# Kernel optimization log

Measured on AMD Instinct MI355X. Metric: run time of the kernel, lower is better.

Reference implementation:

```python
import jax, jax.numpy as jnp
import numpy as np

B, T, C = 4, 4096, 1024
DEGREE, EXPAND = 2, 2
H = EXPAND * C  # selector / inner dim = 2048


def setup_inputs() -> dict:
    key = jax.random.key(0)
    ks = jax.random.split(key, 4)
    sc = lambda d: 1.0 / np.sqrt(d)
    return {
        "x": jax.random.normal(ks[0], (B, T, C), jnp.float32),
        "W_sel": jax.random.normal(ks[1], (C, H), jnp.float32) * sc(C),
        "W_agg": jax.random.normal(ks[2], (C, DEGREE * H), jnp.float32) * sc(C),
        "W_out": jax.random.normal(ks[3], (H, C), jnp.float32) * sc(H),
        "sqk_q": jnp.ones((H,), jnp.float32),
        "sqk_k": jnp.ones((DEGREE * H,), jnp.float32),
    }


def reference(x, W_sel, W_agg, W_out, sqk_q, sqk_k):
    # Selector branch on queries (gated): B,T,H
    s = jax.nn.silu(jnp.einsum('btc,ch->bth', x, W_sel) * sqk_q)
    # Aggregator branch on context: B,T,DEGREE*H
    h = jnp.einsum('btc,cd->btd', x, W_agg) * sqk_k
    chunks = jnp.split(h, DEGREE, axis=-1)
    # Polynomial expansion: sum_{d=1..DEGREE} prod_{k<=d} chunk_k  -> B,T,H
    p = chunks[0]
    poly = p
    for c in chunks[1:]:
        p = p * c
        poly = poly + p
    # Causal masked mean: tril(ones(T,T)) @ poly / row-count == cumsum / arange.
    # Honors the causal structure without materializing the T x T mask.
    denom = jnp.arange(1, T + 1, dtype=poly.dtype)[None, :, None]
    agg = jnp.cumsum(poly, axis=1) / denom  # B,T,H causal running mean
    # Mix selected queries with aggregated polynomial state, project out.
    return jnp.einsum('bth,hc->btc', s * agg, W_out)
```

## Files before the change

### kernel.cpp

```cpp
#include <hip/hip_runtime.h>
#include <hip/hip_bf16.h>
#include <stdint.h>

#define BB 4
#define TT 4096
#define CC 1024
#define HH 2048
#define MM (BB*TT)
#define NCK 32
#define CKS 128

using short8 = __attribute__((ext_vector_type(8))) short;
using f32x4  = __attribute__((ext_vector_type(4))) float;

__device__ __forceinline__ unsigned short f2bf(float f) {
    union { float f; uint32_t u; } v; v.f = f;
    uint32_t r = v.u + 0x7fffu + ((v.u >> 16) & 1u);
    return (unsigned short)(r >> 16);
}
__device__ __forceinline__ float bf2f(unsigned short s) {
    union { uint32_t u; float f; } v; v.u = ((uint32_t)s) << 16;
    return v.f;
}
__device__ __forceinline__ float bf_lo(uint32_t u) {
    union { uint32_t u; float f; } v; v.u = u << 16; return v.f;
}
__device__ __forceinline__ float bf_hi(uint32_t u) {
    union { uint32_t u; float f; } v; v.u = u & 0xFFFF0000u; return v.f;
}
__device__ __forceinline__ uint32_t pack2bf(float lo, float hi) {
    return ((uint32_t)f2bf(lo)) | (((uint32_t)f2bf(hi)) << 16);
}

__global__ void conv_x_kernel(const float* __restrict__ x, unsigned short* __restrict__ xb, int n4) {
    int i = blockIdx.x * blockDim.x + threadIdx.x;
    if (i >= n4) return;
    float4 v = ((const float4*)x)[i];
    ushort4 o;
    o.x = f2bf(v.x); o.y = f2bf(v.y); o.z = f2bf(v.z); o.w = f2bf(v.w);
    ((ushort4*)xb)[i] = o;
}

__global__ void trans_direct_kernel(const float* __restrict__ in, unsigned short* __restrict__ out,
                                    const float* __restrict__ scale, int R, int Cin) {
    __shared__ float tile[32][33];
    int c0 = blockIdx.x * 32, k0 = blockIdx.y * 32;
    int tx = threadIdx.x;
    for (int i = threadIdx.y; i < 32; i += 8) {
        float s = scale ? scale[c0 + tx] : 1.f;
        tile[i][tx] = in[(size_t)(k0 + i) * Cin + c0 + tx] * s;
    }
    __syncthreads();
    for (int i = threadIdx.y; i < 32; i += 8)
        out[(size_t)(c0 + i) * R + k0 + tx] = f2bf(tile[tx][i]);
}

__global__ void trans_pair_kernel(const float* __restrict__ in, unsigned short* __restrict__ out,
                                  const float* __restrict__ scale) {
    __shared__ float tile[32][33];
    int q0 = blockIdx.x * 32, k0 = blockIdx.y * 32;
    int g = q0 >> 5;
    int tx = threadIdx.x;
    int c = (tx < 16) ? (g * 16 + tx) : (2048 + g * 16 + tx - 16);
    float s = scale[c];
    for (int i = threadIdx.y; i < 32; i += 8)
        tile[i][tx] = in[(size_t)(k0 + i) * 4096 + c] * s;
    __syncthreads();
    for (int i = threadIdx.y; i < 32; i += 8)
        out[(size_t)(q0 + i) * 1024 + k0 + tx] = f2bf(tile[tx][i]);
}

__global__ __launch_bounds__(256) void gemm_fused_kernel(
    const unsigned short* __restrict__ A,
    const unsigned short* __restrict__ Bt,
    unsigned short* __restrict__ Sout,
    unsigned short* __restrict__ Pout)
{
    __shared__ __align__(16) unsigned short As[128 * 32];
    __shared__ __align__(16) unsigned short Bs[128 * 32];

    const int mt = blockIdx.x / 48;
    const int nt = blockIdx.x % 48;
    const int m0 = mt << 7, n0 = nt << 7;

    const int tid  = threadIdx.x;
    const int lane = tid & 63;
    const int wave = tid >> 6;
    const int l15  = lane & 15;
    const int quad = lane >> 4;
    const int wm = (wave >> 1) * 64;
    const int wn = (wave & 1) * 64;

    f32x4 acc[4][4];
#pragma unroll
    for (int i = 0; i < 4; i++)
#pragma unroll
        for (int j = 0; j < 4; j++) acc[i][j] = {0.f, 0.f, 0.f, 0.f};

    for (int k0 = 0; k0 < 1024; k0 += 32) {
#pragma unroll
        for (int it = 0; it < 2; it++) {
            int c  = it * 256 + tid;
            int r  = c >> 2;
            int kq = (c & 3) * 8;
            const unsigned short* ga = A  + (size_t)(m0 + r) * 1024 + k0 + kq;
            const unsigned short* gb = Bt + (size_t)(n0 + r) * 1024 + k0 + kq;
            __builtin_amdgcn_global_load_lds(
                (const __attribute__((address_space(1))) void*)ga,
                (__attribute__((address_space(3))) void*)&As[c * 8], 16, 0, 0);
            __builtin_amdgcn_global_load_lds(
                (const __attribute__((address_space(1))) void*)gb,
                (__attribute__((address_space(3))) void*)&Bs[c * 8], 16, 0, 0);
        }
        __syncthreads();

        short8 af[4], bf[4];
#pragma unroll
        for (int i = 0; i < 4; i++)
            af[i] = *(const short8*)&As[(wm + i * 16 + l15) * 32 + quad * 8];
#pragma unroll
        for (int j = 0; j < 4; j++)
            bf[j] = *(const short8*)&Bs[(wn + j * 16 + l15) * 32 + quad * 8];
#pragma unroll
        for (int i = 0; i < 4; i++)
#pragma unroll
            for (int j = 0; j < 4; j++)
                acc[i][j] = __builtin_amdgcn_mfma_f32_16x16x32_bf16(af[i], bf[j], acc[i][j], 0, 0, 0);
        __syncthreads();
    }

    if (nt < 16) {
#pragma unroll
        for (int i = 0; i < 4; i++)
#pragma unroll
            for (int j = 0; j < 4; j++) {
                int col = n0 + wn + j * 16 + l15;
#pragma unroll
                for (int r = 0; r < 4; r++) {
                    int row = m0 + wm + i * 16 + quad * 4 + r;
                    float v = acc[i][j][r];
                    v = v / (1.f + __expf(-v));
                    Sout[(size_t)row * 2048 + col] = f2bf(v);
                }
            }
    } else {
        int pbase = ((n0 - 2048 + wn) >> 1);
#pragma unroll
        for (int i = 0; i < 4; i++)
#pragma unroll
            for (int j = 0; j < 4; j += 2) {
                int pcol = pbase + (j >> 1) * 16 + l15;
#pragma unroll
                for (int r = 0; r < 4; r++) {
                    int row = m0 + wm + i * 16 + quad * 4 + r;
                    float a1 = acc[i][j][r];
                    float a2 = acc[i][j + 1][r];
                    Pout[(size_t)row * 2048 + pcol] = f2bf(a1 * (1.f + a2));
                }
            }
    }
}

__global__ __launch_bounds__(256) void gemm_out_kernel(
    const unsigned short* __restrict__ A,
    const unsigned short* __restrict__ Bt,
    float* __restrict__ Cout)
{
    __shared__ __align__(16) unsigned short As[128 * 32];
    __shared__ __align__(16) unsigned short Bs[128 * 32];

    const int mt = blockIdx.x >> 3;
    const int nt = blockIdx.x & 7;
    const int m0 = mt << 7, n0 = nt << 7;

    const int tid  = threadIdx.x;
    const int lane = tid & 63;
    const int wave = tid >> 6;
    const int l15  = lane & 15;
    const int quad = lane >> 4;
    const int wm = (wave >> 1) * 64;
    const int wn = (wave & 1) * 64;

    f32x4 acc[4][4];
#pragma unroll
    for (int i = 0; i < 4; i++)
#pragma unroll
        for (int j = 0; j < 4; j++) acc[i][j] = {0.f, 0.f, 0.f, 0.f};

    for (int k0 = 0; k0 < 2048; k0 += 32) {
#pragma unroll
        for (int it = 0; it < 2; it++) {
            int c  = it * 256 + tid;
            int r  = c >> 2;
            int kq = (c & 3) * 8;
            const unsigned short* ga = A  + (size_t)(m0 + r) * 2048 + k0 + kq;
            const unsigned short* gb = Bt + (size_t)(n0 + r) * 2048 + k0 + kq;
            __builtin_amdgcn_global_load_lds(
                (const __attribute__((address_space(1))) void*)ga,
                (__attribute__((address_space(3))) void*)&As[c * 8], 16, 0, 0);
            __builtin_amdgcn_global_load_lds(
                (const __attribute__((address_space(1))) void*)gb,
                (__attribute__((address_space(3))) void*)&Bs[c * 8], 16, 0, 0);
        }
        __syncthreads();

        short8 af[4], bf[4];
#pragma unroll
        for (int i = 0; i < 4; i++)
            af[i] = *(const short8*)&As[(wm + i * 16 + l15) * 32 + quad * 8];
#pragma unroll
        for (int j = 0; j < 4; j++)
            bf[j] = *(const short8*)&Bs[(wn + j * 16 + l15) * 32 + quad * 8];
#pragma unroll
        for (int i = 0; i < 4; i++)
#pragma unroll
            for (int j = 0; j < 4; j++)
                acc[i][j] = __builtin_amdgcn_mfma_f32_16x16x32_bf16(af[i], bf[j], acc[i][j], 0, 0, 0);
        __syncthreads();
    }

#pragma unroll
    for (int i = 0; i < 4; i++)
#pragma unroll
        for (int j = 0; j < 4; j++) {
            int col = n0 + wn + j * 16 + l15;
#pragma unroll
            for (int r = 0; r < 4; r++) {
                int row = m0 + wm + i * 16 + quad * 4 + r;
                Cout[(size_t)row * 1024 + col] = acc[i][j][r];
            }
        }
}

__global__ void chunk_sum_kernel(const unsigned short* __restrict__ poly, float* __restrict__ part) {
    int seg = blockIdx.x & 3;
    int ck  = (blockIdx.x >> 2) & (NCK - 1);
    int b   = blockIdx.x >> 7;
    int cp  = seg * 256 + threadIdx.x;
    size_t base = ((size_t)b * TT + (size_t)ck * CKS) * 2048 + cp * 2;
    float s0 = 0.f, s1 = 0.f;
    for (int t = 0; t < CKS; t++) {
        uint32_t v = *(const uint32_t*)&poly[base + (size_t)t * 2048];
        s0 += bf_lo(v);
        s1 += bf_hi(v);
    }
    size_t po = ((size_t)b * NCK + ck) * 2048 + cp * 2;
    part[po] = s0;
    part[po + 1] = s1;
}

__global__ void chunk_scan_kernel(float* __restrict__ part) {
    int idx = blockIdx.x * blockDim.x + threadIdx.x;
    int b = idx >> 11, col = idx & 2047;
    float run = 0.f;
    for (int ck = 0; ck < NCK; ck++) {
        size_t off = ((size_t)b * NCK + ck) * 2048 + col;
        float v = part[off];
        part[off] = run;
        run += v;
    }
}

__global__ void finalize_kernel(unsigned short* __restrict__ poly, const unsigned short* __restrict__ s,
                                const float* __restrict__ part) {
    int seg = blockIdx.x & 3;
    int ck  = (blockIdx.x >> 2) & (NCK - 1);
    int b   = blockIdx.x >> 7;
    int cp  = seg * 256 + threadIdx.x;
    size_t po = ((size_t)b * NCK + ck) * 2048 + cp * 2;
    float run0 = part[po], run1 = part[po + 1];
    size_t base = ((size_t)b * TT + (size_t)ck * CKS) * 2048 + cp * 2;
    for (int t = 0; t < CKS; t++) {
        int tg = ck * CKS + t;
        size_t off = base + (size_t)t * 2048;
        uint32_t pv = *(const uint32_t*)&poly[off];
        run0 += bf_lo(pv);
        run1 += bf_hi(pv);
        float inv = 1.f / (float)(tg + 1);
        uint32_t sv = *(const uint32_t*)&s[off];
        float m0 = bf_lo(sv) * run0 * inv;
        float m1 = bf_hi(sv) * run1 * inv;
        *(uint32_t*)&poly[off] = pack2bf(m0, m1);
    }
}

extern "C" void kernel_launch(void* const* d_in, const int* in_sizes, int n_in,
                              void* d_out, int out_size, void* d_ws, size_t ws_size,
                              hipStream_t stream) {
    const float* x     = (const float*)d_in[0];
    const float* W_sel = (const float*)d_in[1];
    const float* W_agg = (const float*)d_in[2];
    const float* W_out = (const float*)d_in[3];
    const float* sqk_q = (const float*)d_in[4];
    const float* sqk_k = (const float*)d_in[5];
    float* out = (float*)d_out;

    char* ws = (char*)d_ws;
    unsigned short* xb    = (unsigned short*)(ws);
    unsigned short* wallT = (unsigned short*)(ws + 33554432ull);
    unsigned short* woutT = (unsigned short*)(ws + 46137344ull);
    unsigned short* s_b   = (unsigned short*)(ws + 50331648ull);
    unsigned short* poly  = (unsigned short*)(ws + 117440512ull);
    float*          part  = (float*)(ws + 184549376ull);

    dim3 tb(32, 8);
    conv_x_kernel<<<(MM * CC / 4 + 255) / 256, 256, 0, stream>>>(x, xb, MM * CC / 4);
    trans_direct_kernel<<<dim3(HH / 32, CC / 32), tb, 0, stream>>>(W_sel, wallT, sqk_q, CC, HH);
    trans_pair_kernel<<<dim3(4096 / 32, CC / 32), tb, 0, stream>>>(W_agg, wallT + 2048ull * 1024, sqk_k);
    trans_direct_kernel<<<dim3(CC / 32, HH / 32), tb, 0, stream>>>(W_out, woutT, nullptr, HH, CC);

    gemm_fused_kernel<<<(MM / 128) * 48, 256, 0, stream>>>(xb, wallT, s_b, poly);

    chunk_sum_kernel<<<BB * NCK * 4, 256, 0, stream>>>(poly, part);
    chunk_scan_kernel<<<(BB * HH) / 256, 256, 0, stream>>>(part);
    finalize_kernel<<<BB * NCK * 4, 256, 0, stream>>>(poly, s_b, part);

    gemm_out_kernel<<<(MM / 128) * (CC / 128), 256, 0, stream>>>(poly, woutT, out);
}
```

Measured before the change: 541.5 us.

## Fuse prep kernels, compute chunk sums in GEMM epilogue, remap blocks, widen finalize

Merges the x conversion and three weight transposes into one prep launch. Moves the per-chunk column sums into the fused GEMM epilogue through shared-memory atomics, which drops a full re-read of poly. Remaps block indices in both GEMMs so neighbouring blocks share tiles in L2, and widens finalize to four columns per thread. The epilogue sums accumulate unrounded fp32 values rather than bf16 values, and finalize now runs half as many blocks, so it has less parallelism.

```diff
diff --git a/kernel.cpp b/kernel.cpp
--- a/kernel.cpp
+++ b/kernel.cpp
@@ -18,10 +18,6 @@
     uint32_t r = v.u + 0x7fffu + ((v.u >> 16) & 1u);
     return (unsigned short)(r >> 16);
 }
-__device__ __forceinline__ float bf2f(unsigned short s) {
-    union { uint32_t u; float f; } v; v.u = ((uint32_t)s) << 16;
-    return v.f;
-}
 __device__ __forceinline__ float bf_lo(uint32_t u) {
     union { uint32_t u; float f; } v; v.u = u << 16; return v.f;
 }
@@ -32,55 +28,71 @@
     return ((uint32_t)f2bf(lo)) | (((uint32_t)f2bf(hi)) << 16);
 }
 
-__global__ void conv_x_kernel(const float* __restrict__ x, unsigned short* __restrict__ xb, int n4) {
-    int i = blockIdx.x * blockDim.x + threadIdx.x;
-    if (i >= n4) return;
-    float4 v = ((const float4*)x)[i];
-    ushort4 o;
-    o.x = f2bf(v.x); o.y = f2bf(v.y); o.z = f2bf(v.z); o.w = f2bf(v.w);
-    ((ushort4*)xb)[i] = o;
-}
-
-__global__ void trans_direct_kernel(const float* __restrict__ in, unsigned short* __restrict__ out,
-                                    const float* __restrict__ scale, int R, int Cin) {
+__device__ __forceinline__ void trans_body(const float* __restrict__ in, unsigned short* __restrict__ out,
+                                           const float* __restrict__ scale, int R, int Cin,
+                                           int c0, int k0, int tid, float (*tile)[33]) {
+    int tx = tid & 31, ty = tid >> 5;
+    float s = scale ? scale[c0 + tx] : 1.f;
+    for (int i = ty; i < 32; i += 8)
+        tile[i][tx] = in[(size_t)(k0 + i) * Cin + c0 + tx] * s;
+    __syncthreads();
+    for (int i = ty; i < 32; i += 8)
+        out[(size_t)(c0 + i) * R + k0 + tx] = f2bf(tile[tx][i]);
+}
+
+__global__ __launch_bounds__(256) void prep_kernel(
+    const float* __restrict__ x, unsigned short* __restrict__ xb,
+    const float* __restrict__ W_sel, const float* __restrict__ W_agg, const float* __restrict__ W_out,
+    unsigned short* __restrict__ wallT, unsigned short* __restrict__ woutT,
+    const float* __restrict__ sqk_q, const float* __restrict__ sqk_k)
+{
     __shared__ float tile[32][33];
-    int c0 = blockIdx.x * 32, k0 = blockIdx.y * 32;
-    int tx = threadIdx.x;
-    for (int i = threadIdx.y; i < 32; i += 8) {
-        float s = scale ? scale[c0 + tx] : 1.f;
-        tile[i][tx] = in[(size_t)(k0 + i) * Cin + c0 + tx] * s;
-    }
-    __syncthreads();
-    for (int i = threadIdx.y; i < 32; i += 8)
-        out[(size_t)(c0 + i) * R + k0 + tx] = f2bf(tile[tx][i]);
-}
-
-__global__ void trans_pair_kernel(const float* __restrict__ in, unsigned short* __restrict__ out,
-                                  const float* __restrict__ scale) {
-    __shared__ float tile[32][33];
-    int q0 = blockIdx.x * 32, k0 = blockIdx.y * 32;
-    int g = q0 >> 5;
-    int tx = threadIdx.x;
-    int c = (tx < 16) ? (g * 16 + tx) : (2048 + g * 16 + tx - 16);
-    float s = scale[c];
-    for (int i = threadIdx.y; i < 32; i += 8)
-        tile[i][tx] = in[(size_t)(k0 + i) * 4096 + c] * s;
-    __syncthreads();
-    for (int i = threadIdx.y; i < 32; i += 8)
-        out[(size_t)(q0 + i) * 1024 + k0 + tx] = f2bf(tile[tx][i]);
+    int blk = blockIdx.x;
+    int tid = threadIdx.x;
+    if (blk < 16384) {
+        int i = blk * 256 + tid;
+        float4 v = ((const float4*)x)[i];
+        ushort4 o;
+        o.x = f2bf(v.x); o.y = f2bf(v.y); o.z = f2bf(v.z); o.w = f2bf(v.w);
+        ((ushort4*)xb)[i] = o;
+    } else if (blk < 16384 + 2048) {
+        int local = blk - 16384;
+        int c0 = (local & 63) * 32, k0 = (local >> 6) * 32;
+        trans_body(W_sel, wallT, sqk_q, CC, HH, c0, k0, tid, tile);
+    } else if (blk < 16384 + 2048 + 4096) {
+        int local = blk - (16384 + 2048);
+        int q0 = (local & 127) * 32, k0 = (local >> 7) * 32;
+        int g = q0 >> 5;
+        int tx = tid & 31, ty = tid >> 5;
+        int c = (tx < 16) ? (g * 16 + tx) : (2048 + g * 16 + tx - 16);
+        float s = sqk_k[c];
+        for (int i = ty; i < 32; i += 8)
+            tile[i][tx] = W_agg[(size_t)(k0 + i) * 4096 + c] * s;
+        __syncthreads();
+        unsigned short* outp = wallT + 2048ull * 1024;
+        for (int i = ty; i < 32; i += 8)
+            outp[(size_t)(q0 + i) * 1024 + k0 + tx] = f2bf(tile[tx][i]);
+    } else {
+        int local = blk - (16384 + 2048 + 4096);
+        int c0 = (local & 31) * 32, k0 = (local >> 5) * 32;
+        trans_body(W_out, woutT, nullptr, HH, CC, c0, k0, tid, tile);
+    }
 }
 
 __global__ __launch_bounds__(256) void gemm_fused_kernel(
     const unsigned short* __restrict__ A,
     const unsigned short* __restrict__ Bt,
     unsigned short* __restrict__ Sout,
-    unsigned short* __restrict__ Pout)
+    unsigned short* __restrict__ Pout,
+    float* __restrict__ part)
 {
     __shared__ __align__(16) unsigned short As[128 * 32];
     __shared__ __align__(16) unsigned short Bs[128 * 32];
-
-    const int mt = blockIdx.x / 48;
-    const int nt = blockIdx.x % 48;
+    __shared__ float psum[64];
+
+    int blk2 = (blockIdx.x & 7) * 768 + (blockIdx.x >> 3);
+    const int mt = blk2 / 48;
+    const int nt = blk2 % 48;
     const int m0 = mt << 7, n0 = nt << 7;
 
     const int tid  = threadIdx.x;
@@ -144,20 +156,32 @@
                 }
             }
     } else {
+        if (tid < 64) psum[tid] = 0.f;
+        __syncthreads();
         int pbase = ((n0 - 2048 + wn) >> 1);
-#pragma unroll
-        for (int i = 0; i < 4; i++)
+        float lsum0 = 0.f, lsum1 = 0.f;
+#pragma unroll
+        for (int i = 0; i < 4; i++) {
 #pragma unroll
             for (int j = 0; j < 4; j += 2) {
                 int pcol = pbase + (j >> 1) * 16 + l15;
 #pragma unroll
                 for (int r = 0; r < 4; r++) {
                     int row = m0 + wm + i * 16 + quad * 4 + r;
-                    float a1 = acc[i][j][r];
-                    float a2 = acc[i][j + 1][r];
-                    Pout[(size_t)row * 2048 + pcol] = f2bf(a1 * (1.f + a2));
+                    float pv = acc[i][j][r] * (1.f + acc[i][j + 1][r]);
+                    Pout[(size_t)row * 2048 + pcol] = f2bf(pv);
+                    if (j == 0) lsum0 += pv; else lsum1 += pv;
                 }
             }
+        }
+        int pcl = (wn >> 1) + l15;
+        atomicAdd(&psum[pcl], lsum0);
+        atomicAdd(&psum[pcl + 16], lsum1);
+        __syncthreads();
+        if (tid < 64) {
+            int b = m0 >> 12, ck = (m0 & 4095) >> 7;
+            part[((size_t)b * NCK + ck) * 2048 + ((n0 - 2048) >> 1) + tid] = psum[tid];
+        }
     }
 }
 
@@ -169,8 +193,9 @@
     __shared__ __align__(16) unsigned short As[128 * 32];
     __shared__ __align__(16) unsigned short Bs[128 * 32];
 
-    const int mt = blockIdx.x >> 3;
-    const int nt = blockIdx.x & 7;
+    int blk2 = (blockIdx.x & 7) * 128 + (blockIdx.x >> 3);
+    const int mt = blk2 >> 3;
+    const int nt = blk2 & 7;
     const int m0 = mt << 7, n0 = nt << 7;
 
     const int tid  = threadIdx.x;
@@ -232,23 +257,6 @@
         }
 }
 
-__global__ void chunk_sum_kernel(const unsigned short* __restrict__ poly, float* __restrict__ part) {
-    int seg = blockIdx.x & 3;
-    int ck  = (blockIdx.x >> 2) & (NCK - 1);
-    int b   = blockIdx.x >> 7;
-    int cp  = seg * 256 + threadIdx.x;
-    size_t base = ((size_t)b * TT + (size_t)ck * CKS) * 2048 + cp * 2;
-    float s0 = 0.f, s1 = 0.f;
-    for (int t = 0; t < CKS; t++) {
-        uint32_t v = *(const uint32_t*)&poly[base + (size_t)t * 2048];
-        s0 += bf_lo(v);
-        s1 += bf_hi(v);
-    }
-    size_t po = ((size_t)b * NCK + ck) * 2048 + cp * 2;
-    part[po] = s0;
-    part[po + 1] = s1;
-}
-
 __global__ void chunk_scan_kernel(float* __restrict__ part) {
     int idx = blockIdx.x * blockDim.x + threadIdx.x;
     int b = idx >> 11, col = idx & 2047;
@@ -261,26 +269,31 @@
     }
 }
 
-__global__ void finalize_kernel(unsigned short* __restrict__ poly, const unsigned short* __restrict__ s,
-                                const float* __restrict__ part) {
-    int seg = blockIdx.x & 3;
-    int ck  = (blockIdx.x >> 2) & (NCK - 1);
-    int b   = blockIdx.x >> 7;
-    int cp  = seg * 256 + threadIdx.x;
-    size_t po = ((size_t)b * NCK + ck) * 2048 + cp * 2;
-    float run0 = part[po], run1 = part[po + 1];
-    size_t base = ((size_t)b * TT + (size_t)ck * CKS) * 2048 + cp * 2;
+__global__ __launch_bounds__(256) void finalize_kernel(
+    unsigned short* __restrict__ poly, const unsigned short* __restrict__ s,
+    const float* __restrict__ part)
+{
+    int seg = blockIdx.x & 1;
+    int ck  = (blockIdx.x >> 1) & (NCK - 1);
+    int b   = blockIdx.x >> 6;
+    int q   = seg * 256 + threadIdx.x;
+    size_t po = ((size_t)b * NCK + ck) * 2048 + q * 4;
+    float4 run = *(const float4*)&part[po];
+    size_t base = ((size_t)b * TT + (size_t)ck * CKS) * 2048 + q * 4;
     for (int t = 0; t < CKS; t++) {
         int tg = ck * CKS + t;
         size_t off = base + (size_t)t * 2048;
-        uint32_t pv = *(const uint32_t*)&poly[off];
-        run0 += bf_lo(pv);
-        run1 += bf_hi(pv);
+        uint2 pv = *(const uint2*)&poly[off];
+        uint2 sv = *(const uint2*)&s[off];
+        run.x += bf_lo(pv.x);
+        run.y += bf_hi(pv.x);
+        run.z += bf_lo(pv.y);
+        run.w += bf_hi(pv.y);
         float inv = 1.f / (float)(tg + 1);
-        uint32_t sv = *(const uint32_t*)&s[off];
-        float m0 = bf_lo(sv) * run0 * inv;
-        float m1 = bf_hi(sv) * run1 * inv;
-        *(uint32_t*)&poly[off] = pack2bf(m0, m1);
+        uint2 o;
+        o.x = pack2bf(bf_lo(sv.x) * run.x * inv, bf_hi(sv.x) * run.y * inv);
+        o.y = pack2bf(bf_lo(sv.y) * run.z * inv, bf_hi(sv.y) * run.w * inv);
+        *(uint2*)&poly[off] = o;
     }
 }
 
@@ -303,17 +316,13 @@
     unsigned short* poly  = (unsigned short*)(ws + 117440512ull);
     float*          part  = (float*)(ws + 184549376ull);
 
-    dim3 tb(32, 8);
-    conv_x_kernel<<<(MM * CC / 4 + 255) / 256, 256, 0, stream>>>(x, xb, MM * CC / 4);
-    trans_direct_kernel<<<dim3(HH / 32, CC / 32), tb, 0, stream>>>(W_sel, wallT, sqk_q, CC, HH);
-    trans_pair_kernel<<<dim3(4096 / 32, CC / 32), tb, 0, stream>>>(W_agg, wallT + 2048ull * 1024, sqk_k);
-    trans_direct_kernel<<<dim3(CC / 32, HH / 32), tb, 0, stream>>>(W_out, woutT, nullptr, HH, CC);
-
-    gemm_fused_kernel<<<(MM / 128) * 48, 256, 0, stream>>>(xb, wallT, s_b, poly);
-
-    chunk_sum_kernel<<<BB * NCK * 4, 256, 0, stream>>>(poly, part);
+    prep_kernel<<<16384 + 2048 + 4096 + 2048, 256, 0, stream>>>(
+        x, xb, W_sel, W_agg, W_out, wallT, woutT, sqk_q, sqk_k);
+
+    gemm_fused_kernel<<<(MM / 128) * 48, 256, 0, stream>>>(xb, wallT, s_b, poly, part);
+
     chunk_scan_kernel<<<(BB * HH) / 256, 256, 0, stream>>>(part);
-    finalize_kernel<<<BB * NCK * 4, 256, 0, stream>>>(poly, s_b, part);
+    finalize_kernel<<<BB * NCK * 2, 256, 0, stream>>>(poly, s_b, part);
 
     gemm_out_kernel<<<(MM / 128) * (CC / 128), 256, 0, stream>>>(poly, woutT, out);
 }
```

New measurement: 525.9 us. -2.9%, faster.
